# Kernel tuning notes

Hardware: AMD Instinct MI355X
Metric: run time of the kernel (lower is better)

## Reference

```python
import jax, jax.numpy as jnp
import numpy as np

N = 50000      # nodes
E2 = 400000    # undirected edges
E = 2 * E2     # directed edges (each undirected edge in both directions)
DIN = 512      # input feature dim
DH = 128       # MLP hidden
C = 8          # num classes / BP channels


def setup_inputs() -> dict:
    key = jax.random.key(0)
    ks = jax.random.split(key, 9)
    x = jax.random.normal(ks[0], (N, DIN), jnp.float32)
    src0 = jax.random.randint(ks[1], (E2,), 0, N)
    dst0 = jax.random.randint(ks[2], (E2,), 0, N)
    # symmetric directed edge list: row 0 = source j, row 1 = target i
    edge_index = jnp.stack([jnp.concatenate([src0, dst0]),
                            jnp.concatenate([dst0, src0])])
    w0 = jax.random.uniform(ks[3], (E2,), jnp.float32, 0.5, 1.5)
    edge_weight = jnp.concatenate([w0, w0])  # reverse edge shares weight
    # edge_rv[e] = index of the reverse of edge e
    edge_rv = jnp.concatenate([jnp.arange(E2) + E2, jnp.arange(E2)])
    W1 = jax.random.normal(ks[4], (DIN, DH), jnp.float32) * 0.05
    b1 = jnp.zeros((DH,), jnp.float32)
    W2 = jax.random.normal(ks[5], (DH, C), jnp.float32) * 0.05
    b2 = jnp.zeros((C,), jnp.float32)
    param = jax.random.normal(ks[6], (C, C), jnp.float32) * 0.1
    return {"x": x, "edge_index": edge_index, "edge_weight": edge_weight,
            "edge_rv": edge_rv, "W1": W1, "b1": b1, "W2": W2, "b2": b2,
            "param": param, "K": 5}


def log_normalize(log_x):
    return log_x - jax.nn.logsumexp(log_x, axis=-1, keepdims=True)


def reference(x, edge_index, edge_weight, edge_rv, W1, b1, W2, b2, param, K):
    # MLP transform + LogSoftmax -> initial log-beliefs [N, C]
    h = jax.nn.relu(x @ W1 + b1)
    log_b0 = jax.nn.log_softmax(h @ W2 + b2, axis=-1)

    # learn_H=True: logH = logsigmoid(param + param^T), [C, C]
    logH = jax.nn.log_sigmoid(param + param.T)
    src, dst = edge_index[0], edge_index[1]
    # per-edge coupling matrix [E, C, C]
    logC = edge_weight[:, None, None] * logH[None, :, :]

    log_b = log_b0
    log_msg = None
    for _ in range(K):
        x_j = log_b[src]                       # gather source beliefs [E, C]
        if log_msg is not None:
            x_j = x_j - log_msg[edge_rv]       # remove reverse message
        # tropical-semiring matvec in log domain: logsumexp over source channel
        log_msg = log_normalize(jax.nn.logsumexp(x_j[:, :, None] + logC, axis=1))
        agg = jax.ops.segment_sum(log_msg, dst, num_segments=N)  # scatter-add
        log_b = log_normalize(log_b0 + agg)
    return log_b
```

## Files before the change

### kernel.cpp

```cpp
#include <hip/hip_runtime.h>
#include <hip/hip_bf16.h>
#include <hip/hip_fp16.h>
#include <math.h>

#define NN 50000
#define EE 800000
#define E2K 400000
#define DINK 512
#define DHK 128
#define CK 8
#define KIT 5
#define NBLKS 196
#define NPB 32
#define CAP 1024
#define LOG2E 1.4426950408889634f
#define LN2 0.6931471805599453f

typedef __attribute__((ext_vector_type(8))) short short8;
typedef __attribute__((ext_vector_type(4))) float f32x4;

__device__ __forceinline__ unsigned short f2bf(float f) {
    union { float f; unsigned int u; } v;
    v.f = f;
    unsigned int u = v.u;
    unsigned int r = (u + 0x7FFFu + ((u >> 16) & 1u)) >> 16;
    return (unsigned short)r;
}
__device__ __forceinline__ float bfu2f(unsigned int lo16) {
    union { unsigned int u; float f; } v;
    v.u = lo16 << 16;
    return v.f;
}

__global__ __launch_bounds__(256) void prep_kernel(
    const float* __restrict__ W1, const float* __restrict__ param,
    unsigned short* __restrict__ W1t, float* __restrict__ logH,
    int* __restrict__ cnt) {
    if (blockIdx.x < 256) {
        int idx = blockIdx.x * 256 + threadIdx.x;
        int n = idx >> 9;
        int k = idx & 511;
        W1t[idx] = f2bf(W1[(size_t)k * DHK + n]);
    } else if (blockIdx.x == 256) {
        if (threadIdx.x < 64) {
            int t = threadIdx.x;
            int i = t >> 3, j = t & 7;
            float z = param[i * 8 + j] + param[j * 8 + i];
            logH[t] = (fminf(z, 0.0f) - log1pf(expf(-fabsf(z)))) * LOG2E;
        }
    } else {
        int i = (blockIdx.x - 257) * 256 + threadIdx.x;
        if (i < NN) cnt[i] = 0;
    }
}

__global__ __launch_bounds__(256) void mlp_mfma_kernel(
    const float* __restrict__ x, const unsigned short* __restrict__ W1t,
    const float* __restrict__ b1, const float* __restrict__ W2,
    const float* __restrict__ b2, float* __restrict__ logb0) {
    __shared__ unsigned short hs[128 * 136];
    __shared__ float W2s[128 * 8];
    __shared__ float b1s[128];
    __shared__ float b2s[8];

    const int tid = threadIdx.x;
    const int wave = tid >> 6;
    const int lane = tid & 63;
    const int q = lane >> 4;
    const int lm = lane & 15;
    const int wm = wave >> 1, wn = wave & 1;
    const int n0 = blockIdx.x * 128;

    if (tid < 128) b1s[tid] = b1[tid];
    if (tid < 8) b2s[tid] = b2[tid];
    {
        int i = tid * 4;
        *(float4*)&W2s[i] = *(const float4*)&W2[i];
    }
    __syncthreads();

    const float* xptr[4];
#pragma unroll
    for (int mt = 0; mt < 4; ++mt) {
        int r = n0 + wm * 64 + mt * 16 + lm;
        if (r > NN - 1) r = NN - 1;
        xptr[mt] = x + (size_t)r * DINK + q * 8;
    }
    const unsigned short* bptr[4];
#pragma unroll
    for (int nt = 0; nt < 4; ++nt) {
        int c = wn * 64 + nt * 16 + lm;
        bptr[nt] = W1t + (size_t)c * DINK + q * 8;
    }

    f32x4 acc[4][4];
#pragma unroll
    for (int mt = 0; mt < 4; ++mt)
#pragma unroll
        for (int nt = 0; nt < 4; ++nt) acc[mt][nt] = (f32x4){0.f, 0.f, 0.f, 0.f};

    float4 ar[4][2];
    short8 bc[4];
#pragma unroll
    for (int mt = 0; mt < 4; ++mt) {
        ar[mt][0] = *(const float4*)(xptr[mt]);
        ar[mt][1] = *(const float4*)(xptr[mt] + 4);
    }
#pragma unroll
    for (int nt = 0; nt < 4; ++nt) bc[nt] = *(const short8*)(bptr[nt]);

#pragma unroll
    for (int k0 = 32; k0 <= DINK; k0 += 32) {
        float4 ar2[4][2];
        short8 b2f[4];
        if (k0 < DINK) {
#pragma unroll
            for (int mt = 0; mt < 4; ++mt) {
                ar2[mt][0] = *(const float4*)(xptr[mt] + k0);
                ar2[mt][1] = *(const float4*)(xptr[mt] + k0 + 4);
            }
#pragma unroll
            for (int nt = 0; nt < 4; ++nt)
                b2f[nt] = *(const short8*)(bptr[nt] + k0);
        }
        short8 af[4];
#pragma unroll
        for (int mt = 0; mt < 4; ++mt) {
            union { short8 s; __hip_bfloat162 h[4]; } cv;
            cv.h[0] = __float22bfloat162_rn(make_float2(ar[mt][0].x, ar[mt][0].y));
            cv.h[1] = __float22bfloat162_rn(make_float2(ar[mt][0].z, ar[mt][0].w));
            cv.h[2] = __float22bfloat162_rn(make_float2(ar[mt][1].x, ar[mt][1].y));
            cv.h[3] = __float22bfloat162_rn(make_float2(ar[mt][1].z, ar[mt][1].w));
            af[mt] = cv.s;
        }
#pragma unroll
        for (int mt = 0; mt < 4; ++mt)
#pragma unroll
            for (int nt = 0; nt < 4; ++nt)
                acc[mt][nt] = __builtin_amdgcn_mfma_f32_16x16x32_bf16(
                    af[mt], bc[nt], acc[mt][nt], 0, 0, 0);
        if (k0 < DINK) {
#pragma unroll
            for (int mt = 0; mt < 4; ++mt) {
                ar[mt][0] = ar2[mt][0];
                ar[mt][1] = ar2[mt][1];
            }
#pragma unroll
            for (int nt = 0; nt < 4; ++nt) bc[nt] = b2f[nt];
        }
    }

#pragma unroll
    for (int nt = 0; nt < 4; ++nt) {
        int j = wn * 64 + nt * 16 + lm;
        float bj = b1s[j];
#pragma unroll
        for (int mt = 0; mt < 4; ++mt) {
            int rbase = wm * 64 + mt * 16 + q * 4;
#pragma unroll
            for (int r = 0; r < 4; ++r) {
                float h = fmaxf(acc[mt][nt][r] + bj, 0.0f);
                hs[(rbase + r) * 136 + j] = f2bf(h);
            }
        }
    }
    __syncthreads();

    int row = tid >> 1;
    int half = tid & 1;
    const unsigned short* hp = &hs[row * 136 + half * 64];
    float p[8] = {0.f, 0.f, 0.f, 0.f, 0.f, 0.f, 0.f, 0.f};
#pragma unroll
    for (int ch = 0; ch < 8; ++ch) {
        uint4 c4 = *(const uint4*)(hp + ch * 8);
        unsigned int uu[4] = {c4.x, c4.y, c4.z, c4.w};
#pragma unroll
        for (int p2 = 0; p2 < 4; ++p2) {
            float h0 = bfu2f(uu[p2] & 0xFFFFu);
            float h1 = bfu2f(uu[p2] >> 16);
            int j = half * 64 + ch * 8 + p2 * 2;
            const float* w0 = &W2s[j * 8];
            const float* w1 = &W2s[(j + 1) * 8];
#pragma unroll
            for (int c = 0; c < 8; ++c) p[c] = fmaf(h0, w0[c], p[c]);
#pragma unroll
            for (int c = 0; c < 8; ++c) p[c] = fmaf(h1, w1[c], p[c]);
        }
    }
#pragma unroll
    for (int c = 0; c < 8; ++c) p[c] += __shfl_xor(p[c], 1, 64);
    int grow = n0 + row;
    if (half == 0 && grow < NN) {
        float v[8];
        float mx = -1e30f;
#pragma unroll
        for (int c = 0; c < 8; ++c) {
            v[c] = p[c] + b2s[c];
            mx = fmaxf(mx, v[c]);
        }
        float s = 0.0f;
#pragma unroll
        for (int c = 0; c < 8; ++c) s += expf(v[c] - mx);
        float ln = mx + logf(s);
        float4* p0 = (float4*)&logb0[(size_t)grow * 8];
        p0[0] = make_float4(v[0] - ln, v[1] - ln, v[2] - ln, v[3] - ln);
        p0[1] = make_float4(v[4] - ln, v[5] - ln, v[6] - ln, v[7] - ln);
    }
}


__global__ __launch_bounds__(256) void deg_pair_kernel(const int* __restrict__ ei,
                                                       int* __restrict__ cnt) {
    int e = blockIdx.x * 256 + threadIdx.x;
    if (e >= E2K) return;
    int s = ei[e];
    int d = ei[EE + e];
    atomicAdd(&cnt[d], 1);
    atomicAdd(&cnt[s], 1);
}

__global__ __launch_bounds__(256) void scan_partial_kernel(
    const int* __restrict__ cnt, int* __restrict__ partial) {
    __shared__ int sd[256];
    int t = threadIdx.x;
    int i = blockIdx.x * 256 + t;
    sd[t] = (i < NN) ? cnt[i] : 0;
    __syncthreads();
#pragma unroll
    for (int s = 128; s > 0; s >>= 1) {
        if (t < s) sd[t] += sd[t + s];
        __syncthreads();
    }
    if (t == 0) partial[blockIdx.x] = sd[0];
}

__global__ __launch_bounds__(256) void scan_write2_kernel(
    const int* __restrict__ cnt, const int* __restrict__ partial,
    int* __restrict__ off, int* __restrict__ cnt_z) {
    __shared__ int sd[256];
    const int t = threadIdx.x;
    const int b = blockIdx.x;
    sd[t] = (t < NBLKS) ? partial[t] : 0;
    __syncthreads();
#pragma unroll
    for (int s = 1; s < 256; s <<= 1) {
        int a = sd[t];
        int v = (t >= s) ? sd[t - s] : 0;
        __syncthreads();
        sd[t] = a + v;
        __syncthreads();
    }
    const int top = (b > 0) ? sd[b - 1] : 0;
    __syncthreads();
    int i = b * 256 + t;
    int v = (i < NN) ? cnt[i] : 0;
    sd[t] = v;
    __syncthreads();
#pragma unroll
    for (int s = 1; s < 256; s <<= 1) {
        int a = sd[t];
        int w = (t >= s) ? sd[t - s] : 0;
        __syncthreads();
        sd[t] = a + w;
        __syncthreads();
    }
    if (i < NN) {
        off[i] = top + sd[t] - v;
        cnt_z[i] = 0;
    }
    if (i == NN - 1) off[NN] = EE;
}

__global__ __launch_bounds__(256) void pos_zinit_kernel(
    const int* __restrict__ ei, const float* __restrict__ ew,
    const int* __restrict__ off, int* __restrict__ cnt,
    int2* __restrict__ rw, const float* __restrict__ logb0,
    _Float16* __restrict__ z, int E2B) {
    const int t = threadIdx.x;
    if ((int)blockIdx.x < E2B) {
        int e = blockIdx.x * 256 + t;
        if (e >= E2K) return;
        int s = ei[e];
        int d = ei[EE + e];
        int wbits = __float_as_int(ew[e]);
        int pA = off[d] + atomicAdd(&cnt[d], 1);
        int pB = off[s] + atomicAdd(&cnt[s], 1);
        int2 v;
        v.x = pB; v.y = wbits; rw[pA] = v;
        v.x = pA;              rw[pB] = v;
    } else {
        int b = blockIdx.x - E2B;
        int n = b * 32 + (t >> 3);
        int c = t & 7;
        if (n >= NN) return;
        _Float16 v = (_Float16)(logb0[(size_t)n * 8 + c] * LOG2E);
        int j0 = off[n];
        int j1 = off[n + 1];
        for (int j = j0; j < j1; ++j) z[(size_t)j * 8 + c] = v;
    }
}

__device__ __forceinline__ void msg_chunk(
    const int2* __restrict__ rw, const uint4* __restrict__ zprev,
    const float* lH, _Float16* smg, int cb, int ce, int t) {
    for (int j = cb + t; j < ce; j += 256) {
        int2 h = rw[j];
        uint4 zv = zprev[h.x];
        float w = __int_as_float(h.y);
        union { uint4 u; _Float16 hh[8]; } cv;
        cv.u = zv;
        float xj[8];
#pragma unroll
        for (int k = 0; k < 8; ++k) xj[k] = (float)cv.hh[k];
        float mg[8];
#pragma unroll
        for (int c2 = 0; c2 < 8; ++c2) {
            float ssum = 0.0f;
#pragma unroll
            for (int c1 = 0; c1 < 8; ++c1)
                ssum += __builtin_amdgcn_exp2f(fmaf(w, lH[c1 * 8 + c2], xj[c1]));
            mg[c2] = __builtin_amdgcn_logf(ssum);
        }
        union { uint4 u; _Float16 hh[8]; } ov;
#pragma unroll
        for (int k = 0; k < 8; ++k) ov.hh[k] = (_Float16)mg[k];
        *(uint4*)&smg[(j - cb) * 8] = ov.u;
    }
}

__global__ __launch_bounds__(256) void bp_fused_kernel(
    const float* __restrict__ logb0, const int* __restrict__ off,
    const int2* __restrict__ rw, const float* __restrict__ logH,
    const uint4* __restrict__ zprev, _Float16* __restrict__ znext,
    float* __restrict__ out, int last) {
    __shared__ _Float16 smg[CAP * 8];
    __shared__ float lH[64];
    const int t = threadIdx.x;
    if (t < 64) lH[t] = logH[t];

    const int n0 = blockIdx.x * NPB;
    const int nend = (n0 + NPB < NN) ? (n0 + NPB) : NN;
    const int jb0 = off[n0];
    const int jb1 = off[nend];
    const int nl = t >> 3;
    const int c = t & 7;
    const int n = n0 + nl;

    float a = 0.0f;
    int jn0 = 0, jn1 = 0;
    if (n < nend) {
        jn0 = off[n];
        jn1 = off[n + 1];
        a = logb0[(size_t)n * 8 + c] * LOG2E;
    }
    __syncthreads();

    const int single = (jb1 - jb0) <= CAP;

    for (int cb = jb0; cb < jb1; cb += CAP) {
        int ce = (cb + CAP < jb1) ? (cb + CAP) : jb1;
        msg_chunk(rw, zprev, lH, smg, cb, ce, t);
        __syncthreads();
        int lo = (jn0 > cb) ? jn0 : cb;
        int hi = (jn1 < ce) ? jn1 : ce;
        for (int j = lo; j < hi; ++j) a += (float)smg[(j - cb) * 8 + c];
        if (cb + CAP < jb1) __syncthreads();
    }

    float mx = a;
#pragma unroll
    for (int s = 1; s < 8; s <<= 1) mx = fmaxf(mx, __shfl_xor(mx, s, 8));
    float sum = __builtin_amdgcn_exp2f(a - mx);
#pragma unroll
    for (int s = 1; s < 8; s <<= 1) sum += __shfl_xor(sum, s, 8);
    float v = a - (mx + __builtin_amdgcn_logf(sum));
    if (last) {
        if (n < nend) out[(size_t)n * 8 + c] = v * LN2;
        return;
    }

    if (single) {
        if (n < nend) {
            for (int j = jn0; j < jn1; ++j)
                znext[(size_t)j * 8 + c] =
                    (_Float16)(v - (float)smg[(j - jb0) * 8 + c]);
        }
    } else {
        for (int cb = jb0; cb < jb1; cb += CAP) {
            int ce = (cb + CAP < jb1) ? (cb + CAP) : jb1;
            __syncthreads();
            msg_chunk(rw, zprev, lH, smg, cb, ce, t);
            __syncthreads();
            int lo = (jn0 > cb) ? jn0 : cb;
            int hi = (jn1 < ce) ? jn1 : ce;
            for (int j = lo; j < hi; ++j)
                znext[(size_t)j * 8 + c] =
                    (_Float16)(v - (float)smg[(j - cb) * 8 + c]);
        }
    }
}

extern "C" void kernel_launch(void* const* d_in, const int* in_sizes, int n_in,
                              void* d_out, int out_size, void* d_ws, size_t ws_size,
                              hipStream_t stream) {
    const float* x = (const float*)d_in[0];
    const int* ei = (const int*)d_in[1];
    const float* ew = (const float*)d_in[2];
    const float* W1 = (const float*)d_in[4];
    const float* b1 = (const float*)d_in[5];
    const float* W2 = (const float*)d_in[6];
    const float* b2 = (const float*)d_in[7];
    const float* param = (const float*)d_in[8];
    float* out = (float*)d_out;

    float* wsf = (float*)d_ws;
    float* logH = wsf;
    float* logb0 = logH + 64;
    uint4* zA = (uint4*)(logb0 + (size_t)NN * 8);
    uint4* zB = zA + EE;
    int* off = (int*)(zB + EE);
    int2* rw = (int2*)(off + 50004);
    unsigned short* W1t = (unsigned short*)(rw + EE);
    int* cnt = (int*)zB;
    int* partial = cnt + NN;

    const int ZB_ = (NN + 255) / 256;
    prep_kernel<<<257 + ZB_, 256, 0, stream>>>(W1, param, W1t, logH, cnt);
    mlp_mfma_kernel<<<(NN + 127) / 128, 256, 0, stream>>>(x, W1t, b1, W2, b2,
                                                          logb0);

    const int E2B = (E2K + 255) / 256;
    const int AB = (NN + 31) / 32;
    deg_pair_kernel<<<E2B, 256, 0, stream>>>(ei, cnt);
    scan_partial_kernel<<<NBLKS, 256, 0, stream>>>(cnt, partial);
    scan_write2_kernel<<<NBLKS, 256, 0, stream>>>(cnt, partial, off, cnt);
    pos_zinit_kernel<<<E2B + AB, 256, 0, stream>>>(ei, ew, off, cnt, rw, logb0,
                                                   (_Float16*)zA, E2B);

    const int BB = (NN + NPB - 1) / NPB;
    uint4* zs[2] = {zA, zB};
    for (int it = 0; it < KIT; ++it) {
        bp_fused_kernel<<<BB, 256, 0, stream>>>(
            logb0, off, rw, logH, zs[it & 1], (_Float16*)zs[(it + 1) & 1], out,
            it == KIT - 1 ? 1 : 0);
    }
}
```

Measured before the change: 407.3 us.

## Merge scan kernels, fuse z init into edge placement, prefetch in msg loop

Replaces the two-pass block scan with a single kernel where each block recomputes its prefix by summing all preceding counts, and writes a second offset copy that serves as the atomic cursor. Edge placement now also writes the converted initial belief for each placed slot, so the separate per-node z-init pass is removed. The message loop software-prefetches the next edge's record and gathered belief. The redundant prefix summation adds quadratic reads of the count array across blocks, and the prefetch raises register use.

```diff
diff --git a/kernel.cpp b/kernel.cpp
--- a/kernel.cpp
+++ b/kernel.cpp
@@ -219,38 +219,25 @@
     atomicAdd(&cnt[s], 1);
 }
 
-__global__ __launch_bounds__(256) void scan_partial_kernel(
-    const int* __restrict__ cnt, int* __restrict__ partial) {
+__global__ __launch_bounds__(256) void scan_all_kernel(
+    const int* __restrict__ cnt, int* __restrict__ off,
+    int* __restrict__ off2) {
     __shared__ int sd[256];
-    int t = threadIdx.x;
-    int i = blockIdx.x * 256 + t;
-    sd[t] = (i < NN) ? cnt[i] : 0;
+    __shared__ int stop;
+    const int t = threadIdx.x;
+    const int b = blockIdx.x;
+    int acc = 0;
+    for (int i = t; i < b * 256; i += 256) acc += cnt[i];
+    sd[t] = acc;
     __syncthreads();
 #pragma unroll
     for (int s = 128; s > 0; s >>= 1) {
         if (t < s) sd[t] += sd[t + s];
         __syncthreads();
     }
-    if (t == 0) partial[blockIdx.x] = sd[0];
-}
-
-__global__ __launch_bounds__(256) void scan_write2_kernel(
-    const int* __restrict__ cnt, const int* __restrict__ partial,
-    int* __restrict__ off, int* __restrict__ cnt_z) {
-    __shared__ int sd[256];
-    const int t = threadIdx.x;
-    const int b = blockIdx.x;
-    sd[t] = (t < NBLKS) ? partial[t] : 0;
-    __syncthreads();
-#pragma unroll
-    for (int s = 1; s < 256; s <<= 1) {
-        int a = sd[t];
-        int v = (t >= s) ? sd[t - s] : 0;
-        __syncthreads();
-        sd[t] = a + v;
-        __syncthreads();
-    }
-    const int top = (b > 0) ? sd[b - 1] : 0;
+    if (t == 0) stop = sd[0];
+    __syncthreads();
+    const int top = stop;
     __syncthreads();
     int i = b * 256 + t;
     int v = (i < NN) ? cnt[i] : 0;
@@ -265,47 +252,62 @@
         __syncthreads();
     }
     if (i < NN) {
-        off[i] = top + sd[t] - v;
-        cnt_z[i] = 0;
+        int o = top + sd[t] - v;
+        off[i] = o;
+        off2[i] = o;
     }
     if (i == NN - 1) off[NN] = EE;
 }
 
 __global__ __launch_bounds__(256) void pos_zinit_kernel(
     const int* __restrict__ ei, const float* __restrict__ ew,
-    const int* __restrict__ off, int* __restrict__ cnt,
-    int2* __restrict__ rw, const float* __restrict__ logb0,
-    _Float16* __restrict__ z, int E2B) {
-    const int t = threadIdx.x;
-    if ((int)blockIdx.x < E2B) {
-        int e = blockIdx.x * 256 + t;
-        if (e >= E2K) return;
-        int s = ei[e];
-        int d = ei[EE + e];
-        int wbits = __float_as_int(ew[e]);
-        int pA = off[d] + atomicAdd(&cnt[d], 1);
-        int pB = off[s] + atomicAdd(&cnt[s], 1);
-        int2 v;
-        v.x = pB; v.y = wbits; rw[pA] = v;
-        v.x = pA;              rw[pB] = v;
-    } else {
-        int b = blockIdx.x - E2B;
-        int n = b * 32 + (t >> 3);
-        int c = t & 7;
-        if (n >= NN) return;
-        _Float16 v = (_Float16)(logb0[(size_t)n * 8 + c] * LOG2E);
-        int j0 = off[n];
-        int j1 = off[n + 1];
-        for (int j = j0; j < j1; ++j) z[(size_t)j * 8 + c] = v;
-    }
+    int* __restrict__ off2, int2* __restrict__ rw,
+    const float* __restrict__ logb0, _Float16* __restrict__ z) {
+    int e = blockIdx.x * 256 + threadIdx.x;
+    if (e >= E2K) return;
+    int s = ei[e];
+    int d = ei[EE + e];
+    int wbits = __float_as_int(ew[e]);
+    int pA = atomicAdd(&off2[d], 1);
+    int pB = atomicAdd(&off2[s], 1);
+    int2 v;
+    v.x = pB; v.y = wbits; rw[pA] = v;
+    v.x = pA;              rw[pB] = v;
+
+    const float4* pd = (const float4*)&logb0[(size_t)d * 8];
+    float4 d0 = pd[0], d1 = pd[1];
+    union { uint4 u; _Float16 h[8]; } zd;
+    zd.h[0] = (_Float16)(d0.x * LOG2E); zd.h[1] = (_Float16)(d0.y * LOG2E);
+    zd.h[2] = (_Float16)(d0.z * LOG2E); zd.h[3] = (_Float16)(d0.w * LOG2E);
+    zd.h[4] = (_Float16)(d1.x * LOG2E); zd.h[5] = (_Float16)(d1.y * LOG2E);
+    zd.h[6] = (_Float16)(d1.z * LOG2E); zd.h[7] = (_Float16)(d1.w * LOG2E);
+    *(uint4*)&z[(size_t)pA * 8] = zd.u;
+
+    const float4* ps = (const float4*)&logb0[(size_t)s * 8];
+    float4 s0 = ps[0], s1 = ps[1];
+    union { uint4 u; _Float16 h[8]; } zs;
+    zs.h[0] = (_Float16)(s0.x * LOG2E); zs.h[1] = (_Float16)(s0.y * LOG2E);
+    zs.h[2] = (_Float16)(s0.z * LOG2E); zs.h[3] = (_Float16)(s0.w * LOG2E);
+    zs.h[4] = (_Float16)(s1.x * LOG2E); zs.h[5] = (_Float16)(s1.y * LOG2E);
+    zs.h[6] = (_Float16)(s1.z * LOG2E); zs.h[7] = (_Float16)(s1.w * LOG2E);
+    *(uint4*)&z[(size_t)pB * 8] = zs.u;
 }
 
 __device__ __forceinline__ void msg_chunk(
     const int2* __restrict__ rw, const uint4* __restrict__ zprev,
     const float* lH, _Float16* smg, int cb, int ce, int t) {
-    for (int j = cb + t; j < ce; j += 256) {
-        int2 h = rw[j];
-        uint4 zv = zprev[h.x];
+    int j = cb + t;
+    if (j >= ce) return;
+    int2 h = rw[j];
+    uint4 zv = zprev[h.x];
+    while (j < ce) {
+        int jn = j + 256;
+        int2 hn = h;
+        uint4 zn = zv;
+        if (jn < ce) {
+            hn = rw[jn];
+            zn = zprev[hn.x];
+        }
         float w = __int_as_float(h.y);
         union { uint4 u; _Float16 hh[8]; } cv;
         cv.u = zv;
@@ -325,6 +327,9 @@
 #pragma unroll
         for (int k = 0; k < 8; ++k) ov.hh[k] = (_Float16)mg[k];
         *(uint4*)&smg[(j - cb) * 8] = ov.u;
+        j = jn;
+        h = hn;
+        zv = zn;
     }
 }
 
@@ -421,8 +426,8 @@
     int* off = (int*)(zB + EE);
     int2* rw = (int2*)(off + 50004);
     unsigned short* W1t = (unsigned short*)(rw + EE);
+    int* off2 = (int*)(W1t + 65536);
     int* cnt = (int*)zB;
-    int* partial = cnt + NN;
 
     const int ZB_ = (NN + 255) / 256;
     prep_kernel<<<257 + ZB_, 256, 0, stream>>>(W1, param, W1t, logH, cnt);
@@ -430,12 +435,10 @@
                                                           logb0);
 
     const int E2B = (E2K + 255) / 256;
-    const int AB = (NN + 31) / 32;
     deg_pair_kernel<<<E2B, 256, 0, stream>>>(ei, cnt);
-    scan_partial_kernel<<<NBLKS, 256, 0, stream>>>(cnt, partial);
-    scan_write2_kernel<<<NBLKS, 256, 0, stream>>>(cnt, partial, off, cnt);
-    pos_zinit_kernel<<<E2B + AB, 256, 0, stream>>>(ei, ew, off, cnt, rw, logb0,
-                                                   (_Float16*)zA, E2B);
+    scan_all_kernel<<<NBLKS, 256, 0, stream>>>(cnt, off, off2);
+    pos_zinit_kernel<<<E2B, 256, 0, stream>>>(ei, ew, off2, rw, logb0,
+                                              (_Float16*)zA);
 
     const int BB = (NN + NPB - 1) / NPB;
     uint4* zs[2] = {zA, zB};
```

Measured after the change: 431.4 us. +5.9%, slower.
